# Kernel tuning notes

Measured on AMD Instinct MI355X. Metric: run time of the kernel, lower is better.

The kernel has to match this reference:

```python
import jax, jax.numpy as jnp
import numpy as np

N = 50000       # nodes
E = 800000      # edges (avg degree 16)
C_IN = 128
C_OUT = 128
RATIO = 0.5
K = int(np.ceil(RATIO * N))  # static top-k size (single graph)
EPS = 1e-5      # BatchNorm eps


def setup_inputs() -> dict:
    key = jax.random.key(0)
    ks = jax.random.split(key, 12)
    x = jax.random.normal(ks[0], (N, C_IN), jnp.float32)
    edge_index = jax.random.randint(ks[1], (2, E), 0, N, dtype=jnp.int32)
    batch = jnp.zeros((N,), jnp.int32)
    s_in = 1.0 / np.sqrt(C_IN)
    s_out = 1.0 / np.sqrt(C_OUT)
    return {
        "x": x,
        "edge_index": edge_index,
        "batch": batch,
        "lin_w": jax.random.uniform(ks[2], (C_IN, C_OUT), jnp.float32, -s_in, s_in),
        "lin_b": jax.random.uniform(ks[3], (C_OUT,), jnp.float32, -s_in, s_in),
        "bn1_g": jnp.ones((C_OUT,), jnp.float32),
        "bn1_b": jnp.zeros((C_OUT,), jnp.float32),
        "gcn_w": jax.random.uniform(ks[4], (C_OUT, C_OUT), jnp.float32, -s_out, s_out),
        "gcn_b": jnp.zeros((C_OUT,), jnp.float32),
        "bn2_g": jnp.ones((C_OUT,), jnp.float32),
        "bn2_b": jnp.zeros((C_OUT,), jnp.float32),
        "pool_w": jax.random.uniform(ks[5], (C_OUT,), jnp.float32, -s_out, s_out),
    }


def _batchnorm(h, g, b):
    # training-mode BatchNorm1d: biased variance over the node axis
    mu = jnp.mean(h, axis=0)
    var = jnp.mean(jnp.square(h - mu), axis=0)
    return (h - mu) * jax.lax.rsqrt(var + EPS) * g + b


def reference(x, edge_index, batch, lin_w, lin_b, bn1_g, bn1_b,
              gcn_w, gcn_b, bn2_g, bn2_b, pool_w):
    # ---- MLP: Linear + BN + ReLU ----
    h = jax.nn.relu(_batchnorm(x @ lin_w + lin_b, bn1_g, bn1_b))

    # ---- GCNConv with self-loops + symmetric normalization ----
    loops = jnp.arange(N, dtype=edge_index.dtype)
    row = jnp.concatenate([edge_index[0], loops])  # source
    col = jnp.concatenate([edge_index[1], loops])  # target
    hw = h @ gcn_w                                    # [N, C_OUT]
    deg = jax.ops.segment_sum(jnp.ones_like(col, jnp.float32), col, num_segments=N)
    dinv = jnp.where(deg > 0, jax.lax.rsqrt(deg), 0.0)
    norm = dinv[row] * dinv[col]                      # [E+N]
    agg = jax.ops.segment_sum(hw[row] * norm[:, None], col, num_segments=N)
    out = agg + gcn_b

    # ---- BN + ReLU ----
    h2 = jax.nn.relu(_batchnorm(out, bn2_g, bn2_b))

    # ---- TopKPooling (single graph -> static k) ----
    score = jnp.tanh((h2 @ pool_w) / jnp.linalg.norm(pool_w))
    top_score, perm = jax.lax.top_k(score, K)
    x_pool = h2[perm] * top_score[:, None]            # [K, C_OUT]
    batch_new = batch[perm]

    # filter_adj with fixed shape: dropped edges marked -1
    mask = jnp.zeros((N,), bool).at[perm].set(True)
    new_idx = jnp.full((N,), -1, edge_index.dtype).at[perm].set(
        jnp.arange(K, dtype=edge_index.dtype))
    src, dst = edge_index[0], edge_index[1]
    keep = mask[src] & mask[dst]
    ei_new = jnp.where(keep[None, :],
                       jnp.stack([new_idx[src], new_idx[dst]]),
                       jnp.array(-1, edge_index.dtype))
    return x_pool, ei_new, batch_new
```

## Files before the change

### kernel.cpp

```cpp
#include <hip/hip_runtime.h>
#include <hip/hip_bf16.h>

#define NN 50000
#define EE 800000
#define KTOP 25000
#define EPSF 1e-5
#define NB 65536
#define KSHIFT 16

__global__ __launch_bounds__(256, 2) void gemm_bn_stats(const float* __restrict__ A,
                                                        const float* __restrict__ W,
                                                        const float* __restrict__ bias,
                                                        float* __restrict__ Y,
                                                        double* __restrict__ part, int M) {
    __shared__ float Bs[128][128];
    __shared__ float As[32][132];
    int t = threadIdx.x;
    int bm = blockIdx.x * 128;

    const float4* W4 = (const float4*)W;
    float4* Bs4 = (float4*)Bs;
#pragma unroll
    for (int i = 0; i < 16; i++) Bs4[t + i * 256] = W4[t + i * 256];

    float acc[8][8];
#pragma unroll
    for (int i = 0; i < 8; i++)
#pragma unroll
        for (int j = 0; j < 8; j++) acc[i][j] = 0.f;

    int ty = t >> 4;
    int tx = t & 15;

    for (int kc = 0; kc < 4; kc++) {
        __syncthreads();
#pragma unroll
        for (int i = 0; i < 4; i++) {
            int f4 = t + i * 256;
            int r = f4 >> 3, k4 = f4 & 7;
            int row = bm + r;
            float4 v = make_float4(0.f, 0.f, 0.f, 0.f);
            if (row < M) v = *(const float4*)&A[(size_t)row * 128 + kc * 32 + k4 * 4];
            As[k4 * 4 + 0][r] = v.x;
            As[k4 * 4 + 1][r] = v.y;
            As[k4 * 4 + 2][r] = v.z;
            As[k4 * 4 + 3][r] = v.w;
        }
        __syncthreads();
#pragma unroll
        for (int kk = 0; kk < 32; kk++) {
            float4 a0 = *(float4*)&As[kk][ty * 8];
            float4 a1 = *(float4*)&As[kk][ty * 8 + 4];
            float4 b0 = *(float4*)&Bs[kc * 32 + kk][tx * 4];
            float4 b1 = *(float4*)&Bs[kc * 32 + kk][64 + tx * 4];
            float av[8] = {a0.x, a0.y, a0.z, a0.w, a1.x, a1.y, a1.z, a1.w};
            float bv[8] = {b0.x, b0.y, b0.z, b0.w, b1.x, b1.y, b1.z, b1.w};
#pragma unroll
            for (int i = 0; i < 8; i++)
#pragma unroll
                for (int j = 0; j < 8; j++) acc[i][j] += av[i] * bv[j];
        }
    }

    float4 bb0 = *(const float4*)&bias[tx * 4];
    float4 bb1 = *(const float4*)&bias[64 + tx * 4];
    float s[8], s2[8];
#pragma unroll
    for (int j = 0; j < 8; j++) { s[j] = 0.f; s2[j] = 0.f; }
#pragma unroll
    for (int i = 0; i < 8; i++) {
        int row = bm + ty * 8 + i;
        if (row < M) {
            float4 y0, y1;
            y0.x = acc[i][0] + bb0.x; y0.y = acc[i][1] + bb0.y;
            y0.z = acc[i][2] + bb0.z; y0.w = acc[i][3] + bb0.w;
            y1.x = acc[i][4] + bb1.x; y1.y = acc[i][5] + bb1.y;
            y1.z = acc[i][6] + bb1.z; y1.w = acc[i][7] + bb1.w;
            *(float4*)&Y[(size_t)row * 128 + tx * 4] = y0;
            *(float4*)&Y[(size_t)row * 128 + 64 + tx * 4] = y1;
            s[0] += y0.x; s2[0] += y0.x * y0.x;
            s[1] += y0.y; s2[1] += y0.y * y0.y;
            s[2] += y0.z; s2[2] += y0.z * y0.z;
            s[3] += y0.w; s2[3] += y0.w * y0.w;
            s[4] += y1.x; s2[4] += y1.x * y1.x;
            s[5] += y1.y; s2[5] += y1.y * y1.y;
            s[6] += y1.z; s2[6] += y1.z * y1.z;
            s[7] += y1.w; s2[7] += y1.w * y1.w;
        }
    }
    __syncthreads();
    float2* Sred = (float2*)As;
#pragma unroll
    for (int j = 0; j < 8; j++) {
        int col = (j < 4) ? (tx * 4 + j) : (64 + tx * 4 + j - 4);
        Sred[ty * 128 + col] = make_float2(s[j], s2[j]);
    }
    __syncthreads();
    if (t < 128) {
        double S = 0.0, S2 = 0.0;
#pragma unroll
        for (int r = 0; r < 16; r++) {
            float2 v = Sred[r * 128 + t];
            S += (double)v.x;
            S2 += (double)v.y;
        }
        part[((size_t)blockIdx.x * 128 + t) * 2 + 0] = S;
        part[((size_t)blockIdx.x * 128 + t) * 2 + 1] = S2;
    }
}

__global__ __launch_bounds__(256, 2) void gemm_bn_apply(const float* __restrict__ Yin,
                                                        const float* __restrict__ W,
                                                        const float* __restrict__ sc,
                                                        const float* __restrict__ sh,
                                                        const float* __restrict__ dinv,
                                                        float* __restrict__ HWs, int M) {
    __shared__ float Bs[128][128];
    __shared__ float As[32][132];
    int t = threadIdx.x;
    int bm = blockIdx.x * 128;

    const float4* W4 = (const float4*)W;
    float4* Bs4 = (float4*)Bs;
#pragma unroll
    for (int i = 0; i < 16; i++) Bs4[t + i * 256] = W4[t + i * 256];

    float acc[8][8];
#pragma unroll
    for (int i = 0; i < 8; i++)
#pragma unroll
        for (int j = 0; j < 8; j++) acc[i][j] = 0.f;

    int ty = t >> 4;
    int tx = t & 15;

    for (int kc = 0; kc < 4; kc++) {
        __syncthreads();
#pragma unroll
        for (int i = 0; i < 4; i++) {
            int f4 = t + i * 256;
            int r = f4 >> 3, k4 = f4 & 7;
            int row = bm + r;
            int col = kc * 32 + k4 * 4;
            float4 v = make_float4(0.f, 0.f, 0.f, 0.f);
            if (row < M) {
                float4 y = *(const float4*)&Yin[(size_t)row * 128 + col];
                float4 scv = *(const float4*)&sc[col];
                float4 shv = *(const float4*)&sh[col];
                v.x = fmaxf(y.x * scv.x + shv.x, 0.f);
                v.y = fmaxf(y.y * scv.y + shv.y, 0.f);
                v.z = fmaxf(y.z * scv.z + shv.z, 0.f);
                v.w = fmaxf(y.w * scv.w + shv.w, 0.f);
            }
            As[k4 * 4 + 0][r] = v.x;
            As[k4 * 4 + 1][r] = v.y;
            As[k4 * 4 + 2][r] = v.z;
            As[k4 * 4 + 3][r] = v.w;
        }
        __syncthreads();
#pragma unroll
        for (int kk = 0; kk < 32; kk++) {
            float4 a0 = *(float4*)&As[kk][ty * 8];
            float4 a1 = *(float4*)&As[kk][ty * 8 + 4];
            float4 b0 = *(float4*)&Bs[kc * 32 + kk][tx * 4];
            float4 b1 = *(float4*)&Bs[kc * 32 + kk][64 + tx * 4];
            float av[8] = {a0.x, a0.y, a0.z, a0.w, a1.x, a1.y, a1.z, a1.w};
            float bv[8] = {b0.x, b0.y, b0.z, b0.w, b1.x, b1.y, b1.z, b1.w};
#pragma unroll
            for (int i = 0; i < 8; i++)
#pragma unroll
                for (int j = 0; j < 8; j++) acc[i][j] += av[i] * bv[j];
        }
    }
#pragma unroll
    for (int i = 0; i < 8; i++) {
        int row = bm + ty * 8 + i;
        if (row < M) {
            float di = dinv[row];
            float4 o0, o1;
            o0.x = acc[i][0] * di; o0.y = acc[i][1] * di;
            o0.z = acc[i][2] * di; o0.w = acc[i][3] * di;
            o1.x = acc[i][4] * di; o1.y = acc[i][5] * di;
            o1.z = acc[i][6] * di; o1.w = acc[i][7] * di;
            *(float4*)&HWs[(size_t)row * 128 + tx * 4] = o0;
            *(float4*)&HWs[(size_t)row * 128 + 64 + tx * 4] = o1;
        }
    }
}

__global__ __launch_bounds__(256) void bn_finalize(const double* __restrict__ part, int nb,
                                                   const float* __restrict__ g,
                                                   const float* __restrict__ beta,
                                                   float* __restrict__ scale,
                                                   float* __restrict__ shift, int M) {
    int c = blockIdx.x;
    int t = threadIdx.x;
    double s = 0.0, s2 = 0.0;
    for (int b = t; b < nb; b += 256) {
        s += part[((size_t)b * 128 + c) * 2 + 0];
        s2 += part[((size_t)b * 128 + c) * 2 + 1];
    }
    __shared__ double sd[256], sd2[256];
    sd[t] = s;
    sd2[t] = s2;
    __syncthreads();
#pragma unroll
    for (int o = 128; o > 0; o >>= 1) {
        if (t < o) {
            sd[t] += sd[t + o];
            sd2[t] += sd2[t + o];
        }
        __syncthreads();
    }
    if (t == 0) {
        double S = sd[0], S2 = sd2[0];
        double mu = S / (double)M;
        double var = S2 / (double)M - mu * mu;
        double inv = 1.0 / sqrt(var + (double)EPSF);
        scale[c] = (float)((double)g[c] * inv);
        shift[c] = (float)((double)beta[c] - mu * (double)g[c] * inv);
    }
}

__global__ __launch_bounds__(256) void bn_finalize2(const float2* __restrict__ part, int nb,
                                                    const float* __restrict__ g,
                                                    const float* __restrict__ beta,
                                                    float* __restrict__ scale,
                                                    float* __restrict__ shift, int M) {
    int c = blockIdx.x;
    int t = threadIdx.x;
    double s = 0.0, s2 = 0.0;
    for (int b = t; b < nb; b += 256) {
        float2 v = part[(size_t)b * 128 + c];
        s += (double)v.x;
        s2 += (double)v.y;
    }
    __shared__ double sd[256], sd2[256];
    sd[t] = s;
    sd2[t] = s2;
    __syncthreads();
#pragma unroll
    for (int o = 128; o > 0; o >>= 1) {
        if (t < o) {
            sd[t] += sd[t + o];
            sd2[t] += sd2[t + o];
        }
        __syncthreads();
    }
    if (t == 0) {
        double S = sd[0], S2 = sd2[0];
        double mu = S / (double)M;
        double var = S2 / (double)M - mu * mu;
        double inv = 1.0 / sqrt(var + (double)EPSF);
        scale[c] = (float)((double)g[c] * inv);
        shift[c] = (float)((double)beta[c] - mu * (double)g[c] * inv);
    }
}

__global__ __launch_bounds__(256) void count_deg(const int* __restrict__ col,
                                                 int* __restrict__ cnt,
                                                 int* __restrict__ zbase, int zn, int E) {
    int e = blockIdx.x * 256 + threadIdx.x;
    if (e < zn) zbase[e] = 0;
    if (e < E) atomicAdd(&cnt[col[e]], 1);
}

__global__ __launch_bounds__(256) void fill_csr(const int* __restrict__ row,
                                                const int* __restrict__ col,
                                                const int* __restrict__ off,
                                                const int* __restrict__ bsum,
                                                int* __restrict__ cur,
                                                int* __restrict__ csr, int E) {
    int e = blockIdx.x * 256 + threadIdx.x;
    if (e < E) {
        int c = col[e];
        int p = atomicAdd(&cur[c], 1);
        csr[off[c] + bsum[c >> 10] + p] = row[e];
    }
}

__device__ __forceinline__ int waveInclScan(int v, int lane) {
#pragma unroll
    for (int o = 1; o < 64; o <<= 1) {
        int u = __shfl_up(v, o, 64);
        if (lane >= o) v += u;
    }
    return v;
}

__global__ __launch_bounds__(1024) void scan_phase1(const int* __restrict__ in,
                                                    int* __restrict__ out,
                                                    int* __restrict__ bsum,
                                                    float* __restrict__ dinv, int n) {
    int t = threadIdx.x;
    int g = blockIdx.x * 1024 + t;
    int lane = t & 63, wid = t >> 6;
    int v = (g < n) ? in[g] : 0;
    if (dinv && g < n) dinv[g] = (float)(1.0 / sqrt((double)(v + 1)));
    int incl = waveInclScan(v, lane);
    __shared__ int ws[16];
    if (lane == 63) ws[wid] = incl;
    __syncthreads();
    if (t < 16) {
        int x = ws[t];
#pragma unroll
        for (int o = 1; o < 16; o <<= 1) {
            int u = __shfl_up(x, o, 64);
            if (t >= o) x += u;
        }
        ws[t] = x;
    }
    __syncthreads();
    int pre = (wid > 0) ? ws[wid - 1] : 0;
    if (g < n) out[g] = pre + incl - v;
    if (t == 1023) bsum[blockIdx.x] = ws[15];
}

__global__ __launch_bounds__(1024) void scan_phase2(int* __restrict__ bsum, int B) {
    int t = threadIdx.x;
    int lane = t & 63, wid = t >> 6;
    int v = (t < B) ? bsum[t] : 0;
    int incl = waveInclScan(v, lane);
    __shared__ int ws[16];
    if (lane == 63) ws[wid] = incl;
    __syncthreads();
    if (t < 16) {
        int x = ws[t];
#pragma unroll
        for (int o = 1; o < 16; o <<= 1) {
            int u = __shfl_up(x, o, 64);
            if (t >= o) x += u;
        }
        ws[t] = x;
    }
    __syncthreads();
    int pre = (wid > 0) ? ws[wid - 1] : 0;
    if (t < B) bsum[t] = pre + incl - v;
}

__global__ __launch_bounds__(512) void gcn_agg(const float* __restrict__ HWs,
                                               const int* __restrict__ off,
                                               const int* __restrict__ bsum,
                                               const int* __restrict__ csr,
                                               const float* __restrict__ dinv,
                                               const float* __restrict__ gcn_b,
                                               float* __restrict__ OUT,
                                               float2* __restrict__ part32, int M) {
    int t = threadIdx.x;
    int w = t >> 6;
    int lane = t & 63;
    int half = lane >> 5;
    int l32 = lane & 31;
    int i = blockIdx.x * 8 + w;

    const float4* H4 = (const float4*)HWs;
    double a0 = 0.0, a1 = 0.0, a2 = 0.0, a3 = 0.0;

    if (i < M) {
        int o0 = off[i] + bsum[i >> 10];
        int o1 = (i + 1 < M) ? (off[i + 1] + bsum[(i + 1) >> 10]) : EE;
        if (half == 0) {
            float4 sv = H4[(size_t)i * 32 + l32];
            a0 = sv.x; a1 = sv.y; a2 = sv.z; a3 = sv.w;
        }
        int e = o0;
        for (; e + 4 <= o1; e += 4) {
            int sA = csr[e + half];
            int sB = csr[e + 2 + half];
            float4 vA = H4[(size_t)sA * 32 + l32];
            float4 vB = H4[(size_t)sB * 32 + l32];
            a0 += (double)vA.x + (double)vB.x;
            a1 += (double)vA.y + (double)vB.y;
            a2 += (double)vA.z + (double)vB.z;
            a3 += (double)vA.w + (double)vB.w;
        }
        if (e + 2 <= o1) {
            int sA = csr[e + half];
            float4 vA = H4[(size_t)sA * 32 + l32];
            a0 += (double)vA.x; a1 += (double)vA.y;
            a2 += (double)vA.z; a3 += (double)vA.w;
            e += 2;
        }
        if (e < o1 && half == 0) {
            int sA = csr[e];
            float4 vA = H4[(size_t)sA * 32 + l32];
            a0 += (double)vA.x; a1 += (double)vA.y;
            a2 += (double)vA.z; a3 += (double)vA.w;
        }
    }
    a0 += __shfl_down(a0, 32, 64);
    a1 += __shfl_down(a1, 32, 64);
    a2 += __shfl_down(a2, 32, 64);
    a3 += __shfl_down(a3, 32, 64);

    __shared__ float4 sredS[8][32];
    __shared__ float4 sredQ[8][32];
    if (half == 0) {
        if (i < M) {
            double di = (double)dinv[i];
            float4 gb = ((const float4*)gcn_b)[l32];
            float4 y;
            y.x = (float)(a0 * di) + gb.x;
            y.y = (float)(a1 * di) + gb.y;
            y.z = (float)(a2 * di) + gb.z;
            y.w = (float)(a3 * di) + gb.w;
            ((float4*)OUT)[(size_t)i * 32 + l32] = y;
            sredS[w][l32] = y;
            sredQ[w][l32] = make_float4(y.x * y.x, y.y * y.y, y.z * y.z, y.w * y.w);
        } else {
            sredS[w][l32] = make_float4(0.f, 0.f, 0.f, 0.f);
            sredQ[w][l32] = make_float4(0.f, 0.f, 0.f, 0.f);
        }
    }
    __syncthreads();
    if (t < 128) {
        const float* fS = (const float*)sredS;
        const float* fQ = (const float*)sredQ;
        float S = 0.f, S2 = 0.f;
#pragma unroll
        for (int ww = 0; ww < 8; ww++) {
            S += fS[ww * 128 + t];
            S2 += fQ[ww * 128 + t];
        }
        part32[(size_t)blockIdx.x * 128 + t] = make_float2(S, S2);
    }
}

__global__ __launch_bounds__(256) void score_key(const float* __restrict__ Y2,
                                                 const float* __restrict__ sc,
                                                 const float* __restrict__ sh,
                                                 const float* __restrict__ w,
                                                 float* __restrict__ score,
                                                 unsigned* __restrict__ key,
                                                 int* __restrict__ bcnt, int M) {
    int lane = threadIdx.x & 63;
    int wid = threadIdx.x >> 6;
    int gw = blockIdx.x * 4 + wid;
    int nw = gridDim.x * 4;

    float w0 = w[lane], w1 = w[lane + 64];
    float sc0 = sc[lane], sh0 = sh[lane];
    float sc1 = sc[lane + 64], sh1 = sh[lane + 64];

    float nv = w0 * w0 + w1 * w1;
#pragma unroll
    for (int o = 32; o >= 1; o >>= 1) nv += __shfl_xor(nv, o, 64);
    float nrm = sqrtf(nv);

    for (int r = gw; r < M; r += nw) {
        float a = Y2[(size_t)r * 128 + lane];
        float b = Y2[(size_t)r * 128 + lane + 64];
        a = fmaxf(a * sc0 + sh0, 0.f);
        b = fmaxf(b * sc1 + sh1, 0.f);
        float v = a * w0 + b * w1;
#pragma unroll
        for (int o = 32; o >= 1; o >>= 1) v += __shfl_xor(v, o, 64);
        if (lane == 0) {
            score[r] = tanhf(v / nrm);
            unsigned u = __float_as_uint(v);
            unsigned k = (u & 0x80000000u) ? ~u : (u | 0x80000000u);
            key[r] = k;
            atomicAdd(&bcnt[k >> KSHIFT], 1);
        }
    }
}

__global__ __launch_bounds__(256) void bucket_fill(const unsigned* __restrict__ key,
                                                   const int* __restrict__ boff,
                                                   const int* __restrict__ bsum,
                                                   int* __restrict__ bcur,
                                                   uint2* __restrict__ bmem, int M) {
    int i = blockIdx.x * 256 + threadIdx.x;
    if (i < M) {
        unsigned k = key[i];
        int b = k >> KSHIFT;
        int p = atomicAdd(&bcur[b], 1);
        bmem[boff[b] + bsum[b >> 10] + p] = make_uint2(k, (unsigned)i);
    }
}

__global__ __launch_bounds__(256) void rank_pool(const unsigned* __restrict__ key,
                                                 const int* __restrict__ boff,
                                                 const int* __restrict__ bsum,
                                                 const uint2* __restrict__ bmem,
                                                 const float* __restrict__ Y2,
                                                 const float* __restrict__ sc,
                                                 const float* __restrict__ sh,
                                                 const float* __restrict__ score,
                                                 int* __restrict__ nidx,
                                                 float* __restrict__ out0,
                                                 float* __restrict__ out2, int M) {
    __shared__ int lrank[256];
    __shared__ float lscore[256];
    int t = threadIdx.x;
    int base = blockIdx.x * 256;
    int i = base + t;
    int r = 0x7fffffff;
    if (i < M) {
        unsigned ki = key[i];
        int b = ki >> KSHIFT;
        int p0 = boff[b] + bsum[b >> 10];
        int p1 = (b + 1 < NB) ? (boff[b + 1] + bsum[(b + 1) >> 10]) : M;
        r = M - p1;
        for (int p = p0; p < p1; p++) {
            uint2 kj = bmem[p];
            if (kj.x > ki || (kj.x == ki && (int)kj.y < i)) r++;
        }
        nidx[i] = (r < KTOP) ? r : -1;
        lscore[t] = score[i];
    }
    lrank[t] = r;
    __syncthreads();

    int sub = t >> 5;
    int c4 = t & 31;
    float4 scv = *(const float4*)&sc[c4 * 4];
    float4 shv = *(const float4*)&sh[c4 * 4];
    for (int n0 = 0; n0 < 256; n0 += 8) {
        int li = n0 + sub;
        int node = base + li;
        if (node < M) {
            int rr = lrank[li];
            if (rr < KTOP) {
                float s = lscore[li];
                float4 y = *(const float4*)&Y2[(size_t)node * 128 + c4 * 4];
                float4 o;
                o.x = fmaxf(y.x * scv.x + shv.x, 0.f) * s;
                o.y = fmaxf(y.y * scv.y + shv.y, 0.f) * s;
                o.z = fmaxf(y.z * scv.z + shv.z, 0.f) * s;
                o.w = fmaxf(y.w * scv.w + shv.w, 0.f) * s;
                *(float4*)&out0[(size_t)rr * 128 + c4 * 4] = o;
                if (c4 == 0) out2[rr] = 0.0f;
            }
        }
    }
}

__global__ __launch_bounds__(256) void write_edges(const int* __restrict__ row,
                                                   const int* __restrict__ col,
                                                   const int* __restrict__ nidx,
                                                   float* __restrict__ out1, int E) {
    int e = blockIdx.x * 256 + threadIdx.x;
    if (e < E) {
        int a = nidx[row[e]];
        int b = nidx[col[e]];
        bool keep = (a >= 0) && (b >= 0);
        out1[e] = keep ? (float)a : -1.0f;
        out1[E + e] = keep ? (float)b : -1.0f;
    }
}

extern "C" void kernel_launch(void* const* d_in, const int* in_sizes, int n_in,
                              void* d_out, int out_size, void* d_ws, size_t ws_size,
                              hipStream_t stream) {
    const float* x = (const float*)d_in[0];
    const int* ei = (const int*)d_in[1];
    const float* lin_w = (const float*)d_in[3];
    const float* lin_b = (const float*)d_in[4];
    const float* bn1_g = (const float*)d_in[5];
    const float* bn1_b = (const float*)d_in[6];
    const float* gcn_w = (const float*)d_in[7];
    const float* gcn_b = (const float*)d_in[8];
    const float* bn2_g = (const float*)d_in[9];
    const float* bn2_b = (const float*)d_in[10];
    const float* pool_w = (const float*)d_in[11];

    const int* e_row = ei;
    const int* e_col = ei + EE;

    char* ws = (char*)d_ws;
    size_t off_b = 0;
    auto alloc = [&](size_t bytes) -> void* {
        void* p = ws + off_b;
        off_b = (off_b + bytes + 255) & ~(size_t)255;
        return p;
    };
    float* y = (float*)alloc((size_t)NN * 128 * 4);
    float* hws = (float*)alloc((size_t)NN * 128 * 4);
    int* cnt = (int*)alloc(NN * 4);
    int* cur = (int*)alloc(NN * 4);
    int* offs = (int*)alloc((NN + 1) * 4);
    float* dinv = (float*)alloc(NN * 4);
    int* csr = (int*)alloc((size_t)EE * 4);
    float* score = (float*)alloc(NN * 4);
    unsigned* key = (unsigned*)alloc(NN * 4);
    int* nidx = (int*)alloc(NN * 4);
    int* bcnt = (int*)alloc((size_t)NB * 4);
    int* bcur = (int*)alloc((size_t)NB * 4);
    int* boff = (int*)alloc(((size_t)NB + 1) * 4);
    uint2* bmem = (uint2*)alloc((size_t)NN * 8);
    double* part = (double*)alloc((size_t)400 * 128 * 2 * 8);
    float* scale1 = (float*)alloc(128 * 4);
    float* shift1 = (float*)alloc(128 * 4);
    float* scale2 = (float*)alloc(128 * 4);
    float* shift2 = (float*)alloc(128 * 4);
    int* bsumA = (int*)alloc(256 * 4);
    int* bsumB = (int*)alloc(256 * 4);

    float* out0 = (float*)d_out;
    float* out1 = out0 + (size_t)KTOP * 128;
    float* out2 = out1 + (size_t)2 * EE;

    float2* part32 = (float2*)out0;
    int gcn_grid = (NN + 7) / 8;
    int gemm_grid = (NN + 127) / 128;

    hipMemsetAsync(cnt, 0, (size_t)((char*)cur - (char*)cnt) + NN * 4, stream);
    count_deg<<<(EE + 255) / 256, 256, 0, stream>>>(e_col, cnt, bcnt, 2 * NB, EE);
    {
        int B = (NN + 1023) / 1024;
        scan_phase1<<<B, 1024, 0, stream>>>(cnt, offs, bsumA, dinv, NN);
        scan_phase2<<<1, 1024, 0, stream>>>(bsumA, B);
    }
    fill_csr<<<(EE + 255) / 256, 256, 0, stream>>>(e_row, e_col, offs, bsumA, cur, csr, EE);

    gemm_bn_stats<<<gemm_grid, 256, 0, stream>>>(x, lin_w, lin_b, y, part, NN);
    bn_finalize<<<128, 256, 0, stream>>>(part, gemm_grid, bn1_g, bn1_b, scale1, shift1, NN);

    gemm_bn_apply<<<gemm_grid, 256, 0, stream>>>(y, gcn_w, scale1, shift1, dinv, hws, NN);
    gcn_agg<<<gcn_grid, 512, 0, stream>>>(hws, offs, bsumA, csr, dinv, gcn_b, y, part32, NN);

    bn_finalize2<<<128, 256, 0, stream>>>(part32, gcn_grid, bn2_g, bn2_b, scale2, shift2, NN);

    score_key<<<512, 256, 0, stream>>>(y, scale2, shift2, pool_w, score, key, bcnt, NN);
    {
        int B = NB / 1024;
        scan_phase1<<<B, 1024, 0, stream>>>(bcnt, boff, bsumB, nullptr, NB);
        scan_phase2<<<1, 1024, 0, stream>>>(bsumB, B);
    }
    bucket_fill<<<(NN + 255) / 256, 256, 0, stream>>>(key, boff, bsumB, bcur, bmem, NN);
    rank_pool<<<(NN + 255) / 256, 256, 0, stream>>>(key, boff, bsumB, bmem, y, scale2,
                                                    shift2, score, nidx, out0, out2, NN);
    write_edges<<<(EE + 255) / 256, 256, 0, stream>>>(e_row, e_col, nidx, out1, EE);
}
```

Before: 378.8 us.

## Fuse top-k pipeline into one cooperative kernel and stream GEMM weight tiles

Replaces the score, bucket scan, bucket fill, rank/pool and edge-write kernels with a single cooperative persistent kernel that uses grid-wide syncs between phases. The bucket prefix scan is rewritten as a wave scan plus a single-block scan of group sums. The aim is to remove several launch gaps and tail effects. Separately, the two GEMMs now stage the weight matrix per 32-row chunk instead of holding all 128x128 in shared memory, and launch bounds are raised to 4 blocks per SM for more occupancy. The cost is grid.sync overhead and reloading the weights for every K chunk.

```diff
diff --git a/kernel.cpp b/kernel.cpp
--- a/kernel.cpp
+++ b/kernel.cpp
@@ -1,5 +1,8 @@
 #include <hip/hip_runtime.h>
 #include <hip/hip_bf16.h>
+#include <hip/hip_cooperative_groups.h>
+
+namespace cg = cooperative_groups;
 
 #define NN 50000
 #define EE 800000
@@ -7,21 +10,19 @@
 #define EPSF 1e-5
 #define NB 65536
 #define KSHIFT 16
-
-__global__ __launch_bounds__(256, 2) void gemm_bn_stats(const float* __restrict__ A,
+#define TG 768
+
+__global__ __launch_bounds__(256, 4) void gemm_bn_stats(const float* __restrict__ A,
                                                         const float* __restrict__ W,
                                                         const float* __restrict__ bias,
                                                         float* __restrict__ Y,
                                                         double* __restrict__ part, int M) {
-    __shared__ float Bs[128][128];
+    __shared__ float Bsc[32][132];
     __shared__ float As[32][132];
     int t = threadIdx.x;
     int bm = blockIdx.x * 128;
 
     const float4* W4 = (const float4*)W;
-    float4* Bs4 = (float4*)Bs;
-#pragma unroll
-    for (int i = 0; i < 16; i++) Bs4[t + i * 256] = W4[t + i * 256];
 
     float acc[8][8];
 #pragma unroll
@@ -34,6 +35,13 @@
 
     for (int kc = 0; kc < 4; kc++) {
         __syncthreads();
+#pragma unroll
+        for (int i = 0; i < 4; i++) {
+            int f4 = t + i * 256;
+            int r = f4 >> 5, c = f4 & 31;
+            float4 wv = W4[(kc * 32 + r) * 32 + c];
+            *(float4*)&Bsc[r][c * 4] = wv;
+        }
 #pragma unroll
         for (int i = 0; i < 4; i++) {
             int f4 = t + i * 256;
@@ -51,8 +59,8 @@
         for (int kk = 0; kk < 32; kk++) {
             float4 a0 = *(float4*)&As[kk][ty * 8];
             float4 a1 = *(float4*)&As[kk][ty * 8 + 4];
-            float4 b0 = *(float4*)&Bs[kc * 32 + kk][tx * 4];
-            float4 b1 = *(float4*)&Bs[kc * 32 + kk][64 + tx * 4];
+            float4 b0 = *(float4*)&Bsc[kk][tx * 4];
+            float4 b1 = *(float4*)&Bsc[kk][64 + tx * 4];
             float av[8] = {a0.x, a0.y, a0.z, a0.w, a1.x, a1.y, a1.z, a1.w};
             float bv[8] = {b0.x, b0.y, b0.z, b0.w, b1.x, b1.y, b1.z, b1.w};
 #pragma unroll
@@ -109,21 +117,18 @@
     }
 }
 
-__global__ __launch_bounds__(256, 2) void gemm_bn_apply(const float* __restrict__ Yin,
+__global__ __launch_bounds__(256, 4) void gemm_bn_apply(const float* __restrict__ Yin,
                                                         const float* __restrict__ W,
                                                         const float* __restrict__ sc,
                                                         const float* __restrict__ sh,
                                                         const float* __restrict__ dinv,
                                                         float* __restrict__ HWs, int M) {
-    __shared__ float Bs[128][128];
+    __shared__ float Bsc[32][132];
     __shared__ float As[32][132];
     int t = threadIdx.x;
     int bm = blockIdx.x * 128;
 
     const float4* W4 = (const float4*)W;
-    float4* Bs4 = (float4*)Bs;
-#pragma unroll
-    for (int i = 0; i < 16; i++) Bs4[t + i * 256] = W4[t + i * 256];
 
     float acc[8][8];
 #pragma unroll
@@ -136,6 +141,13 @@
 
     for (int kc = 0; kc < 4; kc++) {
         __syncthreads();
+#pragma unroll
+        for (int i = 0; i < 4; i++) {
+            int f4 = t + i * 256;
+            int r = f4 >> 5, c = f4 & 31;
+            float4 wv = W4[(kc * 32 + r) * 32 + c];
+            *(float4*)&Bsc[r][c * 4] = wv;
+        }
 #pragma unroll
         for (int i = 0; i < 4; i++) {
             int f4 = t + i * 256;
@@ -162,8 +174,8 @@
         for (int kk = 0; kk < 32; kk++) {
             float4 a0 = *(float4*)&As[kk][ty * 8];
             float4 a1 = *(float4*)&As[kk][ty * 8 + 4];
-            float4 b0 = *(float4*)&Bs[kc * 32 + kk][tx * 4];
-            float4 b1 = *(float4*)&Bs[kc * 32 + kk][64 + tx * 4];
+            float4 b0 = *(float4*)&Bsc[kk][tx * 4];
+            float4 b1 = *(float4*)&Bsc[kk][64 + tx * 4];
             float av[8] = {a0.x, a0.y, a0.z, a0.w, a1.x, a1.y, a1.z, a1.w};
             float bv[8] = {b0.x, b0.y, b0.z, b0.w, b1.x, b1.y, b1.z, b1.w};
 #pragma unroll
@@ -426,127 +438,162 @@
     }
 }
 
-__global__ __launch_bounds__(256) void score_key(const float* __restrict__ Y2,
-                                                 const float* __restrict__ sc,
-                                                 const float* __restrict__ sh,
-                                                 const float* __restrict__ w,
-                                                 float* __restrict__ score,
-                                                 unsigned* __restrict__ key,
-                                                 int* __restrict__ bcnt, int M) {
-    int lane = threadIdx.x & 63;
-    int wid = threadIdx.x >> 6;
-    int gw = blockIdx.x * 4 + wid;
-    int nw = gridDim.x * 4;
-
-    float w0 = w[lane], w1 = w[lane + 64];
-    float sc0 = sc[lane], sh0 = sh[lane];
-    float sc1 = sc[lane + 64], sh1 = sh[lane + 64];
-
-    float nv = w0 * w0 + w1 * w1;
-#pragma unroll
-    for (int o = 32; o >= 1; o >>= 1) nv += __shfl_xor(nv, o, 64);
-    float nrm = sqrtf(nv);
-
-    for (int r = gw; r < M; r += nw) {
-        float a = Y2[(size_t)r * 128 + lane];
-        float b = Y2[(size_t)r * 128 + lane + 64];
-        a = fmaxf(a * sc0 + sh0, 0.f);
-        b = fmaxf(b * sc1 + sh1, 0.f);
-        float v = a * w0 + b * w1;
-#pragma unroll
-        for (int o = 32; o >= 1; o >>= 1) v += __shfl_xor(v, o, 64);
-        if (lane == 0) {
-            score[r] = tanhf(v / nrm);
-            unsigned u = __float_as_uint(v);
-            unsigned k = (u & 0x80000000u) ? ~u : (u | 0x80000000u);
-            key[r] = k;
-            atomicAdd(&bcnt[k >> KSHIFT], 1);
-        }
-    }
-}
-
-__global__ __launch_bounds__(256) void bucket_fill(const unsigned* __restrict__ key,
-                                                   const int* __restrict__ boff,
-                                                   const int* __restrict__ bsum,
-                                                   int* __restrict__ bcur,
-                                                   uint2* __restrict__ bmem, int M) {
-    int i = blockIdx.x * 256 + threadIdx.x;
-    if (i < M) {
-        unsigned k = key[i];
-        int b = k >> KSHIFT;
-        int p = atomicAdd(&bcur[b], 1);
-        bmem[boff[b] + bsum[b >> 10] + p] = make_uint2(k, (unsigned)i);
-    }
-}
-
-__global__ __launch_bounds__(256) void rank_pool(const unsigned* __restrict__ key,
-                                                 const int* __restrict__ boff,
-                                                 const int* __restrict__ bsum,
-                                                 const uint2* __restrict__ bmem,
-                                                 const float* __restrict__ Y2,
-                                                 const float* __restrict__ sc,
-                                                 const float* __restrict__ sh,
-                                                 const float* __restrict__ score,
-                                                 int* __restrict__ nidx,
-                                                 float* __restrict__ out0,
-                                                 float* __restrict__ out2, int M) {
+__global__ __launch_bounds__(256, 4) void topk_fused(const float* __restrict__ Y2,
+                                                     const float* __restrict__ sc,
+                                                     const float* __restrict__ sh,
+                                                     const float* __restrict__ pw,
+                                                     float* __restrict__ score,
+                                                     unsigned* __restrict__ key,
+                                                     int* __restrict__ bcnt,
+                                                     int* __restrict__ bcur,
+                                                     int* __restrict__ boff,
+                                                     int* __restrict__ gbsum,
+                                                     uint2* __restrict__ bmem,
+                                                     int* __restrict__ nidx,
+                                                     float* __restrict__ out0,
+                                                     float* __restrict__ out1,
+                                                     float* __restrict__ out2,
+                                                     const int* __restrict__ erow,
+                                                     const int* __restrict__ ecol,
+                                                     int M, int E) {
+    cg::grid_group grid = cg::this_grid();
     __shared__ int lrank[256];
     __shared__ float lscore[256];
-    int t = threadIdx.x;
-    int base = blockIdx.x * 256;
-    int i = base + t;
-    int r = 0x7fffffff;
-    if (i < M) {
-        unsigned ki = key[i];
-        int b = ki >> KSHIFT;
-        int p0 = boff[b] + bsum[b >> 10];
-        int p1 = (b + 1 < NB) ? (boff[b + 1] + bsum[(b + 1) >> 10]) : M;
-        r = M - p1;
-        for (int p = p0; p < p1; p++) {
-            uint2 kj = bmem[p];
-            if (kj.x > ki || (kj.x == ki && (int)kj.y < i)) r++;
-        }
-        nidx[i] = (r < KTOP) ? r : -1;
-        lscore[t] = score[i];
-    }
-    lrank[t] = r;
-    __syncthreads();
-
-    int sub = t >> 5;
-    int c4 = t & 31;
-    float4 scv = *(const float4*)&sc[c4 * 4];
-    float4 shv = *(const float4*)&sh[c4 * 4];
-    for (int n0 = 0; n0 < 256; n0 += 8) {
-        int li = n0 + sub;
-        int node = base + li;
-        if (node < M) {
-            int rr = lrank[li];
-            if (rr < KTOP) {
-                float s = lscore[li];
-                float4 y = *(const float4*)&Y2[(size_t)node * 128 + c4 * 4];
-                float4 o;
-                o.x = fmaxf(y.x * scv.x + shv.x, 0.f) * s;
-                o.y = fmaxf(y.y * scv.y + shv.y, 0.f) * s;
-                o.z = fmaxf(y.z * scv.z + shv.z, 0.f) * s;
-                o.w = fmaxf(y.w * scv.w + shv.w, 0.f) * s;
-                *(float4*)&out0[(size_t)rr * 128 + c4 * 4] = o;
-                if (c4 == 0) out2[rr] = 0.0f;
+    __shared__ int ws4[4];
+
+    int t = threadIdx.x;
+    int b = blockIdx.x;
+    int G = gridDim.x;
+    int lane = t & 63;
+    int wid = t >> 6;
+
+    {
+        float w0 = pw[lane], w1 = pw[lane + 64];
+        float sc0 = sc[lane], sh0 = sh[lane];
+        float sc1 = sc[lane + 64], sh1 = sh[lane + 64];
+        float nv = w0 * w0 + w1 * w1;
+#pragma unroll
+        for (int o = 32; o >= 1; o >>= 1) nv += __shfl_xor(nv, o, 64);
+        float nrm = sqrtf(nv);
+        for (int r = b * 4 + wid; r < M; r += G * 4) {
+            float a = Y2[(size_t)r * 128 + lane];
+            float bb = Y2[(size_t)r * 128 + lane + 64];
+            a = fmaxf(a * sc0 + sh0, 0.f);
+            bb = fmaxf(bb * sc1 + sh1, 0.f);
+            float v = a * w0 + bb * w1;
+#pragma unroll
+            for (int o = 32; o >= 1; o >>= 1) v += __shfl_xor(v, o, 64);
+            if (lane == 0) {
+                score[r] = tanhf(v / nrm);
+                unsigned u = __float_as_uint(v);
+                unsigned k = (u & 0x80000000u) ? ~u : (u | 0x80000000u);
+                key[r] = k;
+                atomicAdd(&bcnt[k >> KSHIFT], 1);
             }
         }
     }
-}
-
-__global__ __launch_bounds__(256) void write_edges(const int* __restrict__ row,
-                                                   const int* __restrict__ col,
-                                                   const int* __restrict__ nidx,
-                                                   float* __restrict__ out1, int E) {
-    int e = blockIdx.x * 256 + threadIdx.x;
-    if (e < E) {
-        int a = nidx[row[e]];
-        int b = nidx[col[e]];
-        bool keep = (a >= 0) && (b >= 0);
+    grid.sync();
+
+    {
+        int g0 = b * 4 + wid;
+        if (g0 < (NB >> 6)) {
+            int bb = (g0 << 6) + lane;
+            int v = bcnt[bb];
+            int incl = waveInclScan(v, lane);
+            boff[bb] = incl - v;
+            if (lane == 63) gbsum[g0] = incl;
+        }
+    }
+    grid.sync();
+
+    if (b == 0) {
+        int v0 = gbsum[t * 4 + 0], v1 = gbsum[t * 4 + 1];
+        int v2 = gbsum[t * 4 + 2], v3 = gbsum[t * 4 + 3];
+        int s4 = v0 + v1 + v2 + v3;
+        int incl = waveInclScan(s4, lane);
+        if (lane == 63) ws4[wid] = incl;
+        __syncthreads();
+        int pre = 0;
+#pragma unroll
+        for (int q = 0; q < 4; q++)
+            if (q < wid) pre += ws4[q];
+        int ex = pre + incl - s4;
+        gbsum[t * 4 + 0] = ex;
+        gbsum[t * 4 + 1] = ex + v0;
+        gbsum[t * 4 + 2] = ex + v0 + v1;
+        gbsum[t * 4 + 3] = ex + v0 + v1 + v2;
+    }
+    grid.sync();
+
+    {
+        int g0 = b * 4 + wid;
+        if (g0 < (NB >> 6)) boff[(g0 << 6) + lane] += gbsum[g0];
+    }
+    grid.sync();
+
+    for (int i = b * 256 + t; i < M; i += G * 256) {
+        unsigned k = key[i];
+        int bb = k >> KSHIFT;
+        int p = atomicAdd(&bcur[bb], 1);
+        bmem[boff[bb] + p] = make_uint2(k, (unsigned)i);
+    }
+    grid.sync();
+
+    {
+        int nst = (M + 255) / 256;
+        for (int s = b; s < nst; s += G) {
+            int base = s * 256;
+            int i = base + t;
+            int r = 0x7fffffff;
+            if (i < M) {
+                unsigned ki = key[i];
+                int bb = ki >> KSHIFT;
+                int p0 = boff[bb];
+                int p1 = (bb + 1 < NB) ? boff[bb + 1] : M;
+                r = M - p1;
+                for (int p = p0; p < p1; p++) {
+                    uint2 kj = bmem[p];
+                    if (kj.x > ki || (kj.x == ki && (int)kj.y < i)) r++;
+                }
+                nidx[i] = (r < KTOP) ? r : -1;
+                lscore[t] = score[i];
+            }
+            lrank[t] = r;
+            __syncthreads();
+
+            int sub = t >> 5;
+            int c4 = t & 31;
+            float4 scv = *(const float4*)&sc[c4 * 4];
+            float4 shv = *(const float4*)&sh[c4 * 4];
+            for (int n0 = 0; n0 < 256; n0 += 8) {
+                int li = n0 + sub;
+                int node = base + li;
+                if (node < M) {
+                    int rr = lrank[li];
+                    if (rr < KTOP) {
+                        float sv = lscore[li];
+                        float4 y = *(const float4*)&Y2[(size_t)node * 128 + c4 * 4];
+                        float4 o;
+                        o.x = fmaxf(y.x * scv.x + shv.x, 0.f) * sv;
+                        o.y = fmaxf(y.y * scv.y + shv.y, 0.f) * sv;
+                        o.z = fmaxf(y.z * scv.z + shv.z, 0.f) * sv;
+                        o.w = fmaxf(y.w * scv.w + shv.w, 0.f) * sv;
+                        *(float4*)&out0[(size_t)rr * 128 + c4 * 4] = o;
+                        if (c4 == 0) out2[rr] = 0.0f;
+                    }
+                }
+            }
+            __syncthreads();
+        }
+    }
+    grid.sync();
+
+    for (int e = b * 256 + t; e < E; e += G * 256) {
+        int a = nidx[erow[e]];
+        int bb = nidx[ecol[e]];
+        bool keep = (a >= 0) && (bb >= 0);
         out1[e] = keep ? (float)a : -1.0f;
-        out1[E + e] = keep ? (float)b : -1.0f;
+        out1[E + e] = keep ? (float)bb : -1.0f;
     }
 }
 
@@ -595,7 +642,7 @@
     float* scale2 = (float*)alloc(128 * 4);
     float* shift2 = (float*)alloc(128 * 4);
     int* bsumA = (int*)alloc(256 * 4);
-    int* bsumB = (int*)alloc(256 * 4);
+    int* gbsum = (int*)alloc(1024 * 4);
 
     float* out0 = (float*)d_out;
     float* out1 = out0 + (size_t)KTOP * 128;
@@ -622,14 +669,13 @@
 
     bn_finalize2<<<128, 256, 0, stream>>>(part32, gcn_grid, bn2_g, bn2_b, scale2, shift2, NN);
 
-    score_key<<<512, 256, 0, stream>>>(y, scale2, shift2, pool_w, score, key, bcnt, NN);
     {
-        int B = NB / 1024;
-        scan_phase1<<<B, 1024, 0, stream>>>(bcnt, boff, bsumB, nullptr, NB);
-        scan_phase2<<<1, 1024, 0, stream>>>(bsumB, B);
-    }
-    bucket_fill<<<(NN + 255) / 256, 256, 0, stream>>>(key, boff, bsumB, bcur, bmem, NN);
-    rank_pool<<<(NN + 255) / 256, 256, 0, stream>>>(key, boff, bsumB, bmem, y, scale2,
-                                                    shift2, score, nidx, out0, out2, NN);
-    write_edges<<<(EE + 255) / 256, 256, 0, stream>>>(e_row, e_col, nidx, out1, EE);
-}
+        int Mv = NN, Ev = EE;
+        void* args[] = {(void*)&y,     (void*)&scale2, (void*)&shift2, (void*)&pool_w,
+                        (void*)&score, (void*)&key,    (void*)&bcnt,   (void*)&bcur,
+                        (void*)&boff,  (void*)&gbsum,  (void*)&bmem,   (void*)&nidx,
+                        (void*)&out0,  (void*)&out1,   (void*)&out2,
+                        (void*)&e_row, (void*)&e_col,  (void*)&Mv,     (void*)&Ev};
+        hipLaunchCooperativeKernel((void*)topk_fused, dim3(TG), dim3(256), args, 0, stream);
+    }
+}
```

New measurement: 882.6 us. 2.33x slower.
